# Performance work log

Hardware: AMD Instinct MI355X
Metric: run time of the kernel (lower is better)

## Reference

```python
import jax, jax.numpy as jnp
import numpy as np

# ---- model hyperparameters (match init_kwargs) ----
NUM_INPUT, NUM_HIDDEN, NUM_OUTPUT = 2048, 65536, 512
FAN_OUT = 256
TAU, THRESHOLD = 20.0, 0.3
SPIKE_DELAY = 1  # must be 1 for the one-step-delay scan formulation below
N = NUM_INPUT + NUM_HIDDEN + NUM_OUTPUT
HID_START, OUT_START = NUM_INPUT, NUM_INPUT + NUM_HIDDEN
SURROGATE_SCALE = 25.0


@jax.custom_vjp
def spike(v):
    """Heaviside spike with sigmoid surrogate gradient (SurrogateSpike)."""
    return (v >= THRESHOLD).astype(v.dtype)

def _spike_fwd(v):
    return spike(v), v

def _spike_bwd(v, g):
    s = jax.nn.sigmoid(SURROGATE_SCALE * (v - THRESHOLD))
    return (g * SURROGATE_SCALE * s * (1.0 - s),)

spike.defvjp(_spike_fwd, _spike_bwd)


def make_targets(seed=42):
    """Structured random connectivity (mirrors _generate_random_targets ranges)."""
    rng = np.random.default_rng(seed)
    t = np.empty((N, FAN_OUT), dtype=np.int64)
    # input neurons -> hidden
    t[:NUM_INPUT] = rng.integers(HID_START, OUT_START, size=(NUM_INPUT, FAN_OUT))
    # hidden neurons -> hidden+output, excluding self
    hid = rng.integers(HID_START, N, size=(NUM_HIDDEN, FAN_OUT))
    src = np.arange(HID_START, OUT_START)[:, None]
    R = N - HID_START
    hid = np.where(hid == src, HID_START + (hid - HID_START + 1) % R, hid)
    t[HID_START:OUT_START] = hid
    # output neurons -> hidden
    t[OUT_START:] = rng.integers(HID_START, OUT_START, size=(NUM_OUTPUT, FAN_OUT))
    return jnp.asarray(t, dtype=jnp.int32)


def setup_inputs() -> dict:
    key = jax.random.key(0)
    k1, k2 = jax.random.split(key)
    weights = jax.random.normal(k1, (N, FAN_OUT), dtype=jnp.float32) * 0.3
    input_spikes = jax.random.bernoulli(k2, 0.2, (NUM_INPUT,))
    return {"input_spikes": input_spikes, "weights": weights,
            "targets": make_targets(), "max_timesteps": 50}


def _simulate(input_spikes, weights, targets, max_timesteps):
    decay_base = jnp.exp(jnp.float32(-1.0 / TAU))
    idx = jnp.arange(N)
    flat_targets = targets.reshape(-1)  # [N*FAN_OUT]

    inp = jnp.zeros(N, bool).at[:NUM_INPUT].set(input_spikes)
    pot = jnp.zeros(N, jnp.float32)
    last_update = jnp.zeros(N, jnp.int32)
    has_fired = inp
    strength = jnp.where(inp, 2.0, 0.0).astype(jnp.float32)
    out_times = jnp.full(NUM_OUTPUT, -1, jnp.int32)
    fire_now = inp  # input spikes scheduled on the wheel at t=0

    def step(carry, t):
        pot, last_update, has_fired, strength, fire_now, out_times = carry
        # contributions of spiking sources: spike_strength[src] * weights[src]
        src_val = jnp.where(fire_now, strength, 0.0)                 # [N]
        contrib = (src_val[:, None] * weights).reshape(-1)           # [N*FAN_OUT]
        # neurons that receive at least one spike this step (the 'unique_targets')
        hits = jnp.zeros(N, jnp.float32).at[flat_targets].add(
            jnp.repeat(fire_now.astype(jnp.float32), FAN_OUT))
        is_target = hits > 0
        # lazy retroactive decay only on touched neurons
        dt = (t - last_update).astype(jnp.float32)
        pot = jnp.where(is_target, pot * decay_base ** dt, pot)
        last_update = jnp.where(is_target, t, last_update)
        # scatter-add contributions (zeros for non-firing sources)
        pot = pot.at[flat_targets].add(contrib)
        # spike check with refractory mask
        probs = spike(pot) * (1.0 - has_fired.astype(jnp.float32))
        new_fired = probs > 0.5
        has_fired = has_fired | new_fired
        strength = jnp.where(new_fired, probs, strength)
        out_times = jnp.where(new_fired[OUT_START:] & (out_times < 0), t, out_times)
        # schedule hidden spikes for delivery at t + 1 (spike_delay == 1)
        fire_next = new_fired & (idx < OUT_START)
        # reset membrane of newly fired non-output neurons
        reset = jnp.where(idx >= OUT_START, 0.0, probs)
        pot = pot * (1.0 - reset)
        return (pot, last_update, has_fired, strength, fire_next, out_times), None

    carry = (pot, last_update, has_fired, strength, fire_now, out_times)
    carry, _ = jax.lax.scan(step, carry, jnp.arange(max_timesteps, dtype=jnp.int32))
    pot, last_update, has_fired, strength, _, out_times = carry
    # final decay to end of simulation window
    final_dt = (max_timesteps - last_update).astype(jnp.float32)
    pot = pot * decay_base ** final_dt
    return out_times, pot[OUT_START:]


def reference(input_spikes, weights, targets, max_timesteps):
    out_times, out_pot = _simulate(input_spikes, weights, targets, max_timesteps)
    return out_times, out_pot
```

## Files before the change

kernel.cpp:

```cpp
#include <hip/hip_runtime.h>
#include <math.h>

#define N_TOTAL    68096
#define NUM_INPUT  2048
#define NUM_OUTPUT 512
#define OUT_START  67584
#define FAN_OUT    256
#define THRESH     0.3f
#define T_MAX      50
#define T_BIG      12
#define BM_WORDS   2064
#define LIST_CAP   12288

#define HALF_SZ    33024
#define N_CHUNK    128
#define DENSE_THR  1500
#define DENSE_T_LO 1
#define DENSE_T_HI 3

__global__ __launch_bounds__(256) void init_k(
    const unsigned int* __restrict__ in0,
    float* pot, float* acc, int* last_up, unsigned char* fired,
    int* frontier0, int* cnt, float* out_f, float* decay_tab)
{
    __shared__ int sF, sG;
    const int tid = threadIdx.x;
    if (tid == 0) { sF = 0; sG = 0; }
    __syncthreads();
    for (int k = tid; k < 512; k += 256) {
        unsigned int v = in0[k];
        if (v == 0x3F800000u) atomicAdd(&sF, 1);
        else if (v > 1u)      sG = 1;
    }
    __syncthreads();
    const int mode = (sF >= 8) ? 1 : (sG ? 2 : 0);

    const int i = blockIdx.x * 256 + tid;
    const int lane = tid & 63;
    if (i <= T_MAX) {
        float base = expf(-0.05f);
        decay_tab[i] = (float)pow((double)base, (double)i);
    }
    if (i < NUM_OUTPUT) out_f[i] = -1.0f;
    bool want = false;
    if (i < N_TOTAL) {
        pot[i] = 0.0f;
        acc[i] = 0.0f;
        last_up[i] = 0;
        bool s = false;
        if (i < NUM_INPUT) {
            if (mode == 0)      s = ((const int*)in0)[i] != 0;
            else if (mode == 1) s = ((const float*)in0)[i] != 0.0f;
            else                s = ((const unsigned char*)in0)[i] != 0;
        }
        fired[i] = s ? 1 : 0;
        want = s;
    }
    unsigned long long m = __ballot(want);
    if (m) {
        int leader = __ffsll((long long)m) - 1;
        int base = 0;
        if (lane == leader) base = atomicAdd(&cnt[0], __popcll(m));
        base = __shfl(base, leader, 64);
        if (want) {
            int off = __popcll(m & ((1ull << (unsigned)lane) - 1ull));
            frontier0[base + off] = i;
        }
    }
}

__global__ __launch_bounds__(256) void scatter_k(
    const int* __restrict__ frontier, const int* __restrict__ cnt_cur,
    int* cnt_next,
    const int* __restrict__ targets, const float* __restrict__ weights,
    float* __restrict__ acc, int gate)
{
    if (blockIdx.x == 0 && threadIdx.x == 0) *cnt_next = 0;
    const int fcnt = *cnt_cur;
    if (fcnt >= gate) return;
    const int nq = fcnt * (FAN_OUT / 4);
    const int stride = gridDim.x * 256;
    for (int q = blockIdx.x * 256 + threadIdx.x; q < nq; q += stride) {
        int s  = frontier[q >> 6];
        int j4 = (q & 63) << 2;
        const int base = s * FAN_OUT + j4;
        int4   tg = *(const int4*)  (targets + base);
        float4 wv = *(const float4*)(weights + base);
        float  st = (s < NUM_INPUT) ? 2.0f : 1.0f;
        atomicAdd(&acc[tg.x], st * wv.x);
        atomicAdd(&acc[tg.y], st * wv.y);
        atomicAdd(&acc[tg.z], st * wv.z);
        atomicAdd(&acc[tg.w], st * wv.w);
    }
}

__global__ __launch_bounds__(256) void update_k(
    float* __restrict__ pot, float* __restrict__ acc,
    int* __restrict__ last_up, unsigned char* __restrict__ fired,
    int* __restrict__ frontier_next, int* __restrict__ cnt_next,
    float* __restrict__ out_f, const float* __restrict__ decay_tab, int t,
    const int* __restrict__ cnt_cur, int gate)
{
    if (*cnt_cur >= gate) return;
    const int n = NUM_INPUT + blockIdx.x * 256 + threadIdx.x;
    const int lane = threadIdx.x & 63;
    bool w2 = false;
    float a = acc[n];
    if (a != 0.0f) {
        acc[n] = 0.0f;
        float p = pot[n] * decay_tab[t - last_up[n]] + a;
        last_up[n] = t;
        if (!fired[n] && p >= THRESH) {
            fired[n] = 1;
            if (n < OUT_START) { p = 0.0f; w2 = true; }
            else out_f[n - OUT_START] = (float)t;
        }
        pot[n] = p;
    }
    unsigned long long m = __ballot(w2);
    if (m) {
        int leader = __ffsll((long long)m) - 1;
        int base = 0;
        if (lane == leader) base = atomicAdd(cnt_next, __popcll(m));
        base = __shfl(base, leader, 64);
        if (w2) {
            int off = __popcll(m & ((1ull << (unsigned)lane) - 1ull));
            frontier_next[base + off] = n;
        }
    }
}

__global__ __launch_bounds__(1024) void dense_scatter_k(
    const int* __restrict__ fr, const int* __restrict__ cnt_cur,
    const int* __restrict__ targets, const float* __restrict__ weights,
    float* __restrict__ rep)
{
    const int fcnt = *cnt_cur;
    if (fcnt < DENSE_THR) return;
    __shared__ float lacc[HALF_SZ];
    const int h    = blockIdx.x & 1;
    const int c    = blockIdx.x >> 1;
    const int base = NUM_INPUT + h * HALF_SZ;
    const int tid  = threadIdx.x;
    for (int k = tid; k < HALF_SZ / 4; k += 1024)
        ((float4*)lacc)[k] = make_float4(0.f, 0.f, 0.f, 0.f);
    __syncthreads();
    const int lo = (int)(((long long)fcnt * c)       / N_CHUNK);
    const int hi = (int)(((long long)fcnt * (c + 1)) / N_CHUNK);
    const int nq = (hi - lo) << 6;
    for (int q = tid; q < nq; q += 1024) {
        const int s  = fr[lo + (q >> 6)];
        const int j4 = (q & 63) << 2;
        const int eb = s * FAN_OUT + j4;
        int4   tg = *(const int4*)  (targets + eb);
        float4 wv = *(const float4*)(weights + eb);
        float  st = (s < NUM_INPUT) ? 2.0f : 1.0f;
        int x;
        x = tg.x - base; if ((unsigned)x < HALF_SZ) atomicAdd(&lacc[x], st * wv.x);
        x = tg.y - base; if ((unsigned)x < HALF_SZ) atomicAdd(&lacc[x], st * wv.y);
        x = tg.z - base; if ((unsigned)x < HALF_SZ) atomicAdd(&lacc[x], st * wv.z);
        x = tg.w - base; if ((unsigned)x < HALF_SZ) atomicAdd(&lacc[x], st * wv.w);
    }
    __syncthreads();
    float4* out = (float4*)(rep + (size_t)((c << 1) + h) * HALF_SZ);
    for (int k = tid; k < HALF_SZ / 4; k += 1024) out[k] = ((float4*)lacc)[k];
}

__global__ __launch_bounds__(1024) void dense_update_k(
    const float* __restrict__ rep, const int* __restrict__ cnt_cur,
    float* __restrict__ pot, int* __restrict__ last_up,
    unsigned char* __restrict__ fired,
    int* __restrict__ frontier_next, int* __restrict__ cnt_next,
    float* __restrict__ out_f, const float* __restrict__ decay_tab, int t)
{
    const int fcnt = *cnt_cur;
    if (fcnt < DENSE_THR) return;
    const int g = blockIdx.x * 1024 + threadIdx.x;
    const int lane = threadIdx.x & 63;
    bool w2 = false;
    const int n = NUM_INPUT + g;
    if (g < 2 * HALF_SZ) {
        const int h   = (g < HALF_SZ) ? 1 : 2;
        const int hh  = h - 1 ? 1 : 0;
        const int idx = g - hh * HALF_SZ;
        const float* p0 = rep + (size_t)hh * HALF_SZ + idx;
        float a0 = 0.f, a1 = 0.f, a2 = 0.f, a3 = 0.f;
        #pragma unroll 4
        for (int c = 0; c < N_CHUNK; c += 4) {
            a0 += p0[(size_t)((c + 0) << 1) * HALF_SZ];
            a1 += p0[(size_t)((c + 1) << 1) * HALF_SZ];
            a2 += p0[(size_t)((c + 2) << 1) * HALF_SZ];
            a3 += p0[(size_t)((c + 3) << 1) * HALF_SZ];
        }
        float a = (a0 + a1) + (a2 + a3);
        if (a != 0.0f) {
            float p = pot[n] * decay_tab[t - last_up[n]] + a;
            last_up[n] = t;
            if (!fired[n] && p >= THRESH) {
                fired[n] = 1;
                if (n < OUT_START) { p = 0.0f; w2 = true; }
                else out_f[n - OUT_START] = (float)t;
            }
            pot[n] = p;
        }
    }
    unsigned long long m = __ballot(w2);
    if (m) {
        int leader = __ffsll((long long)m) - 1;
        int base = 0;
        if (lane == leader) base = atomicAdd(cnt_next, __popcll(m));
        base = __shfl(base, leader, 64);
        if (w2) {
            int off = __popcll(m & ((1ull << (unsigned)lane) - 1ull));
            frontier_next[base + off] = n;
        }
    }
}

__global__ __launch_bounds__(1024) void tail_k(
    float* __restrict__ pot, float* __restrict__ acc,
    int* __restrict__ last_up, unsigned char* __restrict__ fired,
    int* __restrict__ fr0, int* __restrict__ fr1, int* __restrict__ cnt,
    const int* __restrict__ targets, const float* __restrict__ weights,
    float* __restrict__ out_f, const float* __restrict__ decay_tab)
{
    __shared__ unsigned bm[BM_WORDS];
    __shared__ int      lst[LIST_CAP];
    __shared__ int      lcnt, ovf;
    __shared__ float    sdecay[T_MAX + 1];
    const int tid = threadIdx.x;
    if (tid <= T_MAX) sdecay[tid] = decay_tab[tid];

    for (int t = T_BIG; t < T_MAX; ++t) {
        const int cur = t & 1, nxt = cur ^ 1;
        for (int k = tid; k < BM_WORDS; k += 1024) bm[k] = 0u;
        if (tid == 0) { lcnt = 0; ovf = 0; cnt[nxt] = 0; }
        __syncthreads();
        const int fcnt = cnt[cur];
        if (fcnt == 0) break;
        const int* fr  = (cur == 0) ? fr0 : fr1;
        int*       frn = (cur == 0) ? fr1 : fr0;

        const int nq = fcnt * (FAN_OUT / 4);
        for (int q = tid; q < nq; q += 1024) {
            int s  = fr[q >> 6];
            int j4 = (q & 63) << 2;
            const int base = s * FAN_OUT + j4;
            int4   tg = *(const int4*)  (targets + base);
            float4 wv = *(const float4*)(weights + base);
            float  st = (s < NUM_INPUT) ? 2.0f : 1.0f;
            #define EDGE(TG, WV) do {                                         \
                atomicAdd(&acc[TG], st * (WV));                               \
                int b = (TG) - NUM_INPUT;                                     \
                unsigned bit = 1u << (b & 31);                                \
                unsigned old = atomicOr(&bm[b >> 5], bit);                    \
                if (!(old & bit)) {                                           \
                    int p_ = atomicAdd(&lcnt, 1);                             \
                    if (p_ < LIST_CAP) lst[p_] = (TG); else ovf = 1;          \
                } } while (0)
            EDGE(tg.x, wv.x); EDGE(tg.y, wv.y);
            EDGE(tg.z, wv.z); EDGE(tg.w, wv.w);
            #undef EDGE
        }
        __syncthreads();

        const int M = lcnt;
        const bool full = (ovf != 0);
        const int lo = full ? (NUM_INPUT + tid) : tid;
        const int hi = full ? N_TOTAL : M;
        for (int k = lo; k < hi; k += 1024) {
            const int n = full ? k : lst[k];
            float a = __hip_atomic_load(&acc[n], __ATOMIC_RELAXED,
                                        __HIP_MEMORY_SCOPE_AGENT);
            if (a != 0.0f) {
                __hip_atomic_store(&acc[n], 0.0f, __ATOMIC_RELAXED,
                                   __HIP_MEMORY_SCOPE_AGENT);
                float p = pot[n] * sdecay[t - last_up[n]] + a;
                last_up[n] = t;
                if (!fired[n] && p >= THRESH) {
                    fired[n] = 1;
                    if (n < OUT_START) {
                        p = 0.0f;
                        int pos = atomicAdd(&cnt[nxt], 1);
                        frn[pos] = n;
                    } else out_f[n - OUT_START] = (float)t;
                }
                pot[n] = p;
            }
        }
        __syncthreads();
    }

    __syncthreads();
    for (int i = tid; i < NUM_OUTPUT; i += 1024) {
        int n = OUT_START + i;
        out_f[NUM_OUTPUT + i] = pot[n] * sdecay[T_MAX - last_up[n]];
    }
}

extern "C" void kernel_launch(void* const* d_in, const int* in_sizes, int n_in,
                              void* d_out, int out_size, void* d_ws, size_t ws_size,
                              hipStream_t stream) {
    const void*  in_spikes = d_in[0];
    const float* weights   = (const float*)d_in[1];
    const int*   targets   = (const int*)d_in[2];
    float*       out_f     = (float*)d_out;

    char* w = (char*)d_ws;
    int*   cnt       = (int*)w;
    float* decay_tab = (float*)(w + 256);
    float* pot       = (float*)(w + 512);
    float* acc       = pot + N_TOTAL;
    int*   last_up   = (int*)(acc + N_TOTAL);
    int*   fr0       = last_up + N_TOTAL;
    int*   fr1       = fr0 + N_TOTAL;
    unsigned char* fired = (unsigned char*)(fr1 + N_TOTAL);
    size_t base_bytes = (size_t)((char*)(fired + N_TOTAL) - w);
    size_t rep_off    = (base_bytes + 255) & ~(size_t)255;
    float* rep        = (float*)(w + rep_off);
    size_t need       = rep_off + (size_t)N_CHUNK * 2 * HALF_SZ * 4;
    const bool dense_ok = ws_size >= need;

    hipMemsetAsync(cnt, 0, 16, stream);
    init_k<<<266, 256, 0, stream>>>((const unsigned int*)in_spikes,
                                    pot, acc, last_up, fired,
                                    fr0, cnt, out_f, decay_tab);

    int* fr[2] = {fr0, fr1};
    for (int t = 0; t < T_BIG; ++t) {
        const int cur = t & 1, nxt = cur ^ 1;
        const bool dstep = dense_ok && t >= DENSE_T_LO && t <= DENSE_T_HI;
        const int gate = dstep ? DENSE_THR : 0x7fffffff;
        scatter_k<<<512, 256, 0, stream>>>(fr[cur], &cnt[cur], &cnt[nxt],
                                           targets, weights, acc, gate);
        if (dstep) {
            dense_scatter_k<<<2 * N_CHUNK, 1024, 0, stream>>>(
                fr[cur], &cnt[cur], targets, weights, rep);
            dense_update_k<<<65, 1024, 0, stream>>>(
                rep, &cnt[cur], pot, last_up, fired,
                fr[nxt], &cnt[nxt], out_f, decay_tab, t);
        }
        update_k<<<258, 256, 0, stream>>>(pot, acc, last_up, fired,
                                          fr[nxt], &cnt[nxt], out_f,
                                          decay_tab, t, &cnt[cur], gate);
    }
    tail_k<<<1, 1024, 0, stream>>>(pot, acc, last_up, fired, fr0, fr1, cnt,
                                   targets, weights, out_f, decay_tab);
}
```

Before: 308.9 us.

## Merge sparse and dense step paths into two kernels per timestep

Sparse atomic scatter and dense LDS-replica scatter are folded into one kernel that picks its path at runtime from the frontier count, and the two update kernels are merged the same way. This halves kernel launches per step and removes the fixed timestep window for the dense path. The dense path now scales its replica chunk count to the frontier size, so fewer partial sums are written and reduced. Fewer big steps run before the tail kernel and the dense threshold is raised. The sparse path now runs in 1024-thread blocks that reserve a large LDS array, which may lower occupancy. The workspace size check for the replica buffer was also removed.

After: 377.5 us. 22.2% more time.

```diff
diff --git a/kernel.cpp b/kernel.cpp
--- a/kernel.cpp
+++ b/kernel.cpp
@@ -5,18 +5,17 @@
 #define NUM_INPUT  2048
 #define NUM_OUTPUT 512
 #define OUT_START  67584
+#define N_TGT      66048
 #define FAN_OUT    256
 #define THRESH     0.3f
 #define T_MAX      50
-#define T_BIG      12
+#define T_BIG      10
 #define BM_WORDS   2064
 #define LIST_CAP   12288
 
 #define HALF_SZ    33024
 #define N_CHUNK    128
-#define DENSE_THR  1500
-#define DENSE_T_LO 1
-#define DENSE_T_HI 3
+#define DENSE_THR  2000
 
 __global__ __launch_bounds__(256) void init_k(
     const unsigned int* __restrict__ in0,
@@ -69,84 +68,47 @@
     }
 }
 
-__global__ __launch_bounds__(256) void scatter_k(
-    const int* __restrict__ frontier, const int* __restrict__ cnt_cur,
+__global__ __launch_bounds__(1024) void step_scatter_k(
+    const int* __restrict__ fr, const int* __restrict__ cnt_cur,
     int* cnt_next,
     const int* __restrict__ targets, const float* __restrict__ weights,
-    float* __restrict__ acc, int gate)
+    float* __restrict__ acc, float* __restrict__ rep)
 {
-    if (blockIdx.x == 0 && threadIdx.x == 0) *cnt_next = 0;
+    __shared__ float lacc[HALF_SZ];
     const int fcnt = *cnt_cur;
-    if (fcnt >= gate) return;
-    const int nq = fcnt * (FAN_OUT / 4);
-    const int stride = gridDim.x * 256;
-    for (int q = blockIdx.x * 256 + threadIdx.x; q < nq; q += stride) {
-        int s  = frontier[q >> 6];
-        int j4 = (q & 63) << 2;
-        const int base = s * FAN_OUT + j4;
-        int4   tg = *(const int4*)  (targets + base);
-        float4 wv = *(const float4*)(weights + base);
-        float  st = (s < NUM_INPUT) ? 2.0f : 1.0f;
-        atomicAdd(&acc[tg.x], st * wv.x);
-        atomicAdd(&acc[tg.y], st * wv.y);
-        atomicAdd(&acc[tg.z], st * wv.z);
-        atomicAdd(&acc[tg.w], st * wv.w);
-    }
-}
-
-__global__ __launch_bounds__(256) void update_k(
-    float* __restrict__ pot, float* __restrict__ acc,
-    int* __restrict__ last_up, unsigned char* __restrict__ fired,
-    int* __restrict__ frontier_next, int* __restrict__ cnt_next,
-    float* __restrict__ out_f, const float* __restrict__ decay_tab, int t,
-    const int* __restrict__ cnt_cur, int gate)
-{
-    if (*cnt_cur >= gate) return;
-    const int n = NUM_INPUT + blockIdx.x * 256 + threadIdx.x;
-    const int lane = threadIdx.x & 63;
-    bool w2 = false;
-    float a = acc[n];
-    if (a != 0.0f) {
-        acc[n] = 0.0f;
-        float p = pot[n] * decay_tab[t - last_up[n]] + a;
-        last_up[n] = t;
-        if (!fired[n] && p >= THRESH) {
-            fired[n] = 1;
-            if (n < OUT_START) { p = 0.0f; w2 = true; }
-            else out_f[n - OUT_START] = (float)t;
-        }
-        pot[n] = p;
-    }
-    unsigned long long m = __ballot(w2);
-    if (m) {
-        int leader = __ffsll((long long)m) - 1;
-        int base = 0;
-        if (lane == leader) base = atomicAdd(cnt_next, __popcll(m));
-        base = __shfl(base, leader, 64);
-        if (w2) {
-            int off = __popcll(m & ((1ull << (unsigned)lane) - 1ull));
-            frontier_next[base + off] = n;
-        }
-    }
-}
-
-__global__ __launch_bounds__(1024) void dense_scatter_k(
-    const int* __restrict__ fr, const int* __restrict__ cnt_cur,
-    const int* __restrict__ targets, const float* __restrict__ weights,
-    float* __restrict__ rep)
-{
-    const int fcnt = *cnt_cur;
-    if (fcnt < DENSE_THR) return;
-    __shared__ float lacc[HALF_SZ];
+    const int tid  = threadIdx.x;
+    if (blockIdx.x == 0 && tid == 0) *cnt_next = 0;
+    if (fcnt == 0) return;
+
+    if (fcnt < DENSE_THR) {
+        const int nq = fcnt * (FAN_OUT / 4);
+        const int stride = gridDim.x * 1024;
+        for (int q = blockIdx.x * 1024 + tid; q < nq; q += stride) {
+            int s  = fr[q >> 6];
+            int j4 = (q & 63) << 2;
+            const int base = s * FAN_OUT + j4;
+            int4   tg = *(const int4*)  (targets + base);
+            float4 wv = *(const float4*)(weights + base);
+            float  st = (s < NUM_INPUT) ? 2.0f : 1.0f;
+            atomicAdd(&acc[tg.x], st * wv.x);
+            atomicAdd(&acc[tg.y], st * wv.y);
+            atomicAdd(&acc[tg.z], st * wv.z);
+            atomicAdd(&acc[tg.w], st * wv.w);
+        }
+        return;
+    }
+
+    int chunks = fcnt >> 7;
+    if (chunks > N_CHUNK) chunks = N_CHUNK;
+    const int c = blockIdx.x >> 1;
+    if (c >= chunks) return;
     const int h    = blockIdx.x & 1;
-    const int c    = blockIdx.x >> 1;
     const int base = NUM_INPUT + h * HALF_SZ;
-    const int tid  = threadIdx.x;
     for (int k = tid; k < HALF_SZ / 4; k += 1024)
         ((float4*)lacc)[k] = make_float4(0.f, 0.f, 0.f, 0.f);
     __syncthreads();
-    const int lo = (int)(((long long)fcnt * c)       / N_CHUNK);
-    const int hi = (int)(((long long)fcnt * (c + 1)) / N_CHUNK);
+    const int lo = (int)(((long long)fcnt * c)       / chunks);
+    const int hi = (int)(((long long)fcnt * (c + 1)) / chunks);
     const int nq = (hi - lo) << 6;
     for (int q = tid; q < nq; q += 1024) {
         const int s  = fr[lo + (q >> 6)];
@@ -166,33 +128,33 @@
     for (int k = tid; k < HALF_SZ / 4; k += 1024) out[k] = ((float4*)lacc)[k];
 }
 
-__global__ __launch_bounds__(1024) void dense_update_k(
+__global__ __launch_bounds__(1024) void step_update_k(
     const float* __restrict__ rep, const int* __restrict__ cnt_cur,
-    float* __restrict__ pot, int* __restrict__ last_up,
-    unsigned char* __restrict__ fired,
+    float* __restrict__ pot, float* __restrict__ acc,
+    int* __restrict__ last_up, unsigned char* __restrict__ fired,
     int* __restrict__ frontier_next, int* __restrict__ cnt_next,
     float* __restrict__ out_f, const float* __restrict__ decay_tab, int t)
 {
     const int fcnt = *cnt_cur;
-    if (fcnt < DENSE_THR) return;
+    if (fcnt == 0) return;
     const int g = blockIdx.x * 1024 + threadIdx.x;
     const int lane = threadIdx.x & 63;
     bool w2 = false;
     const int n = NUM_INPUT + g;
-    if (g < 2 * HALF_SZ) {
-        const int h   = (g < HALF_SZ) ? 1 : 2;
-        const int hh  = h - 1 ? 1 : 0;
-        const int idx = g - hh * HALF_SZ;
-        const float* p0 = rep + (size_t)hh * HALF_SZ + idx;
-        float a0 = 0.f, a1 = 0.f, a2 = 0.f, a3 = 0.f;
-        #pragma unroll 4
-        for (int c = 0; c < N_CHUNK; c += 4) {
-            a0 += p0[(size_t)((c + 0) << 1) * HALF_SZ];
-            a1 += p0[(size_t)((c + 1) << 1) * HALF_SZ];
-            a2 += p0[(size_t)((c + 2) << 1) * HALF_SZ];
-            a3 += p0[(size_t)((c + 3) << 1) * HALF_SZ];
-        }
-        float a = (a0 + a1) + (a2 + a3);
+    if (g < N_TGT) {
+        float a = 0.0f;
+        if (fcnt < DENSE_THR) {
+            a = acc[n];
+            if (a != 0.0f) acc[n] = 0.0f;
+        } else {
+            int chunks = fcnt >> 7;
+            if (chunks > N_CHUNK) chunks = N_CHUNK;
+            const int hh  = (g >= HALF_SZ) ? 1 : 0;
+            const int idx = g - hh * HALF_SZ;
+            const float* p0 = rep + (size_t)hh * HALF_SZ + idx;
+            for (int c = 0; c < chunks; ++c)
+                a += p0[(size_t)(c << 1) * HALF_SZ];
+        }
         if (a != 0.0f) {
             float p = pot[n] * decay_tab[t - last_up[n]] + a;
             last_up[n] = t;
@@ -318,8 +280,6 @@
     size_t base_bytes = (size_t)((char*)(fired + N_TOTAL) - w);
     size_t rep_off    = (base_bytes + 255) & ~(size_t)255;
     float* rep        = (float*)(w + rep_off);
-    size_t need       = rep_off + (size_t)N_CHUNK * 2 * HALF_SZ * 4;
-    const bool dense_ok = ws_size >= need;
 
     hipMemsetAsync(cnt, 0, 16, stream);
     init_k<<<266, 256, 0, stream>>>((const unsigned int*)in_spikes,
@@ -329,20 +289,11 @@
     int* fr[2] = {fr0, fr1};
     for (int t = 0; t < T_BIG; ++t) {
         const int cur = t & 1, nxt = cur ^ 1;
-        const bool dstep = dense_ok && t >= DENSE_T_LO && t <= DENSE_T_HI;
-        const int gate = dstep ? DENSE_THR : 0x7fffffff;
-        scatter_k<<<512, 256, 0, stream>>>(fr[cur], &cnt[cur], &cnt[nxt],
-                                           targets, weights, acc, gate);
-        if (dstep) {
-            dense_scatter_k<<<2 * N_CHUNK, 1024, 0, stream>>>(
-                fr[cur], &cnt[cur], targets, weights, rep);
-            dense_update_k<<<65, 1024, 0, stream>>>(
-                rep, &cnt[cur], pot, last_up, fired,
-                fr[nxt], &cnt[nxt], out_f, decay_tab, t);
-        }
-        update_k<<<258, 256, 0, stream>>>(pot, acc, last_up, fired,
-                                          fr[nxt], &cnt[nxt], out_f,
-                                          decay_tab, t, &cnt[cur], gate);
+        step_scatter_k<<<2 * N_CHUNK, 1024, 0, stream>>>(
+            fr[cur], &cnt[cur], &cnt[nxt], targets, weights, acc, rep);
+        step_update_k<<<65, 1024, 0, stream>>>(
+            rep, &cnt[cur], pot, acc, last_up, fired,
+            fr[nxt], &cnt[nxt], out_f, decay_tab, t);
     }
     tail_k<<<1, 1024, 0, stream>>>(pot, acc, last_up, fired, fr0, fr1, cnt,
                                    targets, weights, out_f, decay_tab);
```
